# Kernel optimization log

Measured on AMD Instinct MI355X. Metric: run time of the kernel, lower is better.

Reference implementation:

```python
import jax, jax.numpy as jnp
import numpy as np

N_NODES = 20000   # N
N_EDGES = 320000  # E (avg degree 16)
T_STEPS = 16      # T
IN_FEATS = 1      # F
HG = 64           # hidden_g
HT = 128          # hidden_t
LN_EPS = 1e-5


def _layer_norm(x, g, b):
    mu = jnp.mean(x, axis=-1, keepdims=True)
    var = jnp.mean((x - mu) ** 2, axis=-1, keepdims=True)
    return (x - mu) * jax.lax.rsqrt(var + LN_EPS) * g + b


def setup_inputs() -> dict:
    key = jax.random.key(0)
    k = jax.random.split(key, 16)
    r = lambda i, shape, s: jax.random.normal(k[i], shape, jnp.float32) * s
    return dict(
        x_seq=jax.random.normal(k[0], (1, T_STEPS, N_NODES, IN_FEATS), jnp.float32),
        edge_index=jax.random.randint(k[1], (2, N_EDGES), 0, N_NODES, dtype=jnp.int32),
        # SAGEConv layer 0: lin_l (aggregated neighbors, has bias) + lin_r (root)
        W_l0=r(2, (IN_FEATS, HG), 0.5), W_r0=r(3, (IN_FEATS, HG), 0.5), b0=jnp.zeros((HG,), jnp.float32),
        ln0_g=jnp.ones((HG,), jnp.float32), ln0_b=jnp.zeros((HG,), jnp.float32),
        # SAGEConv layer 1
        W_l1=r(4, (HG, HG), 0.1), W_r1=r(5, (HG, HG), 0.1), b1=jnp.zeros((HG,), jnp.float32),
        ln1_g=jnp.ones((HG,), jnp.float32), ln1_b=jnp.zeros((HG,), jnp.float32),
        # GRU (torch layout: gates r,z,n stacked along first dim)
        gru_Wih=r(6, (3 * HT, HG), 0.05), gru_Whh=r(7, (3 * HT, HT), 0.05),
        gru_bih=jnp.zeros((3 * HT,), jnp.float32), gru_bhh=jnp.zeros((3 * HT,), jnp.float32),
        # head
        head_W=r(8, (HT, 1), 0.05), head_b=jnp.zeros((1,), jnp.float32),
    )


def reference(x_seq, edge_index, W_l0, W_r0, b0, ln0_g, ln0_b,
              W_l1, W_r1, b1, ln1_g, ln1_b,
              gru_Wih, gru_Whh, gru_bih, gru_bhh, head_W, head_b):
    src, dst = edge_index[0], edge_index[1]
    # in-degree for mean aggregation (clamped to 1, like PyG mean aggr on isolated nodes)
    deg = jnp.clip(jax.ops.segment_sum(jnp.ones((N_EDGES,), jnp.float32), dst,
                                       num_segments=N_NODES), 1.0)[:, None]

    def sage(x, Wl, Wr, b):
        # mean over incoming neighbors, then lin_l(aggr) + lin_r(root)
        agg = jax.ops.segment_sum(x[src], dst, num_segments=N_NODES) / deg
        return agg @ Wl + x @ Wr + b

    def stack(xt):  # xt: (N, F) -> (N, HG); dropout is identity in eval mode
        h = jax.nn.relu(_layer_norm(sage(xt, W_l0, W_r0, b0), ln0_g, ln0_b))
        h = jax.nn.relu(_layer_norm(sage(h, W_l1, W_r1, b1), ln1_g, ln1_b))
        return h

    X = x_seq[0]  # (T, N, F), B == 1
    # scan over timesteps (matches the per-t Python loop, bounds peak memory)
    _, H = jax.lax.scan(lambda c, xt: (c, stack(xt)), None, X)  # H: (T, N, HG)

    def gru_step(h, xt):  # torch GRU cell; batch = N nodes
        gi = xt @ gru_Wih.T + gru_bih
        gh = h @ gru_Whh.T + gru_bhh
        ir, iz, inn = jnp.split(gi, 3, axis=-1)
        hr, hz, hn = jnp.split(gh, 3, axis=-1)
        r = jax.nn.sigmoid(ir + hr)
        z = jax.nn.sigmoid(iz + hz)
        n = jnp.tanh(inn + r * hn)
        return (1.0 - z) * n + z * h, None

    h0 = jnp.zeros((N_NODES, HT), x_seq.dtype)
    hT, _ = jax.lax.scan(gru_step, h0, H)
    y = (hT @ head_W + head_b)[:, 0]  # (N,)
    return y
```

## Files before the change

### kernel.cpp

```cpp
#include <hip/hip_runtime.h>
#include <math.h>

#define NN 20000
#define NE 320000
#define TS 16
#define HG 64
#define HTT 128
#define NG 384
#define LN_EPS 1e-5f
#define ASTR 1032

typedef __attribute__((ext_vector_type(8))) _Float16 f16x8;
typedef __attribute__((ext_vector_type(4))) float f32x4;

__device__ __forceinline__ float wave_sum64(float v) {
  #pragma unroll
  for (int off = 32; off > 0; off >>= 1) v += __shfl_xor(v, off, 64);
  return v;
}
__device__ __forceinline__ float quad_sum16(float v) {
  #pragma unroll
  for (int off = 1; off < 16; off <<= 1) v += __shfl_xor(v, off, 64);
  return v;
}
__device__ __forceinline__ float fast_sigmoid(float x) {
  return __builtin_amdgcn_rcpf(1.f + __expf(-x));
}
__device__ __forceinline__ float fast_tanh(float x) {
  float e = __expf(-2.f * fabsf(x));
  float th = (1.f - e) * __builtin_amdgcn_rcpf(1.f + e);
  return copysignf(th, x);
}

__global__ __launch_bounds__(256) void k_setup(
    const float* __restrict__ x_seq, float* __restrict__ xT,
    const float* __restrict__ Wih, _Float16* __restrict__ WihF,
    const float* __restrict__ Whh, _Float16* __restrict__ WhhF,
    const float* __restrict__ Wl1, const float* __restrict__ Wr1,
    _Float16* __restrict__ Wchi, _Float16* __restrict__ Wclo,
    const float* __restrict__ Wl0, const float* __restrict__ Wr0,
    const float* __restrict__ b0, const float* __restrict__ g0,
    const float* __restrict__ be0, float* __restrict__ P,
    int* __restrict__ cnt, _Float16* __restrict__ h0r) {
  int gid = blockIdx.x * 256 + threadIdx.x;
  int stride = gridDim.x * 256;
  for (int i = gid; i < NN * TS; i += stride) {
    int t = i / NN, n = i - t * NN;
    xT[n * 16 + t] = x_seq[i];
  }
  for (int i = gid; i < NG * HG; i += stride) WihF[i] = (_Float16)Wih[i];
  for (int i = gid; i < NG * HTT; i += stride) WhhF[i] = (_Float16)Whh[i];
  for (int i = gid; i < HG * 128; i += stride) {
    int n = i >> 7, k = i & 127;
    float x = (k < HG) ? Wl1[k * HG + n] : Wr1[(k - HG) * HG + n];
    _Float16 h = (_Float16)x;
    Wchi[i] = h;
    Wclo[i] = (_Float16)(x - (float)h);
  }
  for (int i = gid; i < NN; i += stride) cnt[i] = 0;
  for (int i = gid; i < 1024; i += stride) h0r[(size_t)NN * 1024 + i] = (_Float16)0.f;
  if (blockIdx.x == 0 && threadIdx.x < 64) {
    int f = threadIdx.x;
    float u = Wl0[f], v = Wr0[f], c = b0[f], g = g0[f];
    float um = wave_sum64(u) * (1.f / 64.f);
    float vm = wave_sum64(v) * (1.f / 64.f);
    float cm = wave_sum64(c) * (1.f / 64.f);
    float uc = u - um, vc = v - vm, cc = c - cm;
    float muu = wave_sum64(uc * uc) * (1.f / 64.f);
    float mvv = wave_sum64(vc * vc) * (1.f / 64.f);
    float mcc = wave_sum64(cc * cc) * (1.f / 64.f);
    float muv = wave_sum64(uc * vc) * (1.f / 64.f);
    float muc = wave_sum64(uc * cc) * (1.f / 64.f);
    float mvc = wave_sum64(vc * cc) * (1.f / 64.f);
    P[f] = uc * g; P[64 + f] = vc * g; P[128 + f] = cc * g; P[192 + f] = be0[f];
    if (f == 0) {
      P[256] = muu; P[257] = mvv; P[258] = mcc;
      P[259] = muv; P[260] = muc; P[261] = mvc;
    }
  }
}

__global__ void k_hist(const int* __restrict__ dst, int* cnt) {
  int e = blockIdx.x * blockDim.x + threadIdx.x;
  if (e < NE) atomicAdd(&cnt[dst[e]], 1);
}

__global__ void k_scan(int* cnt, int* row_ptr, float* deg_inv) {
  __shared__ int s[1024];
  const int PER = 20;
  int tid = threadIdx.x;
  int base = tid * PER;
  int vloc[PER], dloc[PER];
  int sum = 0;
  #pragma unroll
  for (int j = 0; j < PER; j++) {
    int n = base + j;
    int d = (n < NN) ? cnt[n] : 0;
    vloc[j] = sum;
    dloc[j] = d;
    sum += d;
  }
  s[tid] = sum;
  __syncthreads();
  for (int off = 1; off < 1024; off <<= 1) {
    int t = (tid >= off) ? s[tid - off] : 0;
    __syncthreads();
    s[tid] += t;
    __syncthreads();
  }
  int excl = s[tid] - sum;
  #pragma unroll
  for (int j = 0; j < PER; j++) {
    int n = base + j;
    if (n < NN) {
      int rp = excl + vloc[j];
      row_ptr[n] = rp;
      cnt[n] = rp;
      int d = dloc[j];
      deg_inv[n] = 1.0f / (float)((d > 1) ? d : 1);
    }
  }
  if (tid == 1023) row_ptr[NN] = s[1023];
}

__global__ void k_fill(const int* __restrict__ src, const int* __restrict__ dst,
                       int* cursor, int* col) {
  int e = blockIdx.x * blockDim.x + threadIdx.x;
  if (e < NE) {
    int p = atomicAdd(&cursor[dst[e]], 1);
    col[p] = src[e];
  }
}

__global__ __launch_bounds__(256) void k_h0_fused(
    const float* __restrict__ xT,
    const int* __restrict__ row_ptr, const int* __restrict__ col,
    const float* __restrict__ deg_inv,
    const float* __restrict__ P,
    _Float16* __restrict__ h0r) {
  int lane = threadIdx.x & 63;
  int n = blockIdx.x * 4 + (threadIdx.x >> 6);
  int grp = lane >> 4, tl = lane & 15;
  int beg = row_ptr[n];
  int deg = row_ptr[n + 1] - beg;
  float s0 = 0.f, s1 = 0.f;
  int iters = (deg + 7) >> 3;
  for (int it = 0; it < iters; it++) {
    int e0 = it * 8 + grp, e1 = it * 8 + 4 + grp;
    bool v0 = e0 < deg, v1 = e1 < deg;
    int i0 = v0 ? e0 : 0, i1 = v1 ? e1 : 0;
    int c0 = col[beg + i0];
    int c1 = col[beg + i1];
    float x0 = xT[c0 * 16 + tl];
    float x1 = xT[c1 * 16 + tl];
    s0 += v0 ? x0 : 0.f;
    s1 += v1 ? x1 : 0.f;
  }
  float s = s0 + s1;
  s += __shfl_xor(s, 16, 64);
  s += __shfl_xor(s, 32, 64);
  float aggv = s * deg_inv[n];
  float xv = xT[n * 16 + tl];
  float muu = P[256], mvv = P[257], mcc = P[258];
  float muv = P[259], muc = P[260], mvc = P[261];
  #pragma unroll
  for (int half = 0; half < 2; half++) {
    int c = lane + half * 64;
    int t = c >> 3, f8 = (c & 7) * 8;
    float a = __shfl(aggv, t, 64);
    float x = __shfl(xv, t, 64);
    float var = a * a * muu + x * x * mvv + mcc
              + 2.f * (a * x * muv + a * muc + x * mvc);
    float rstd = rsqrtf(var + LN_EPS);
    f16x8 o;
    #pragma unroll
    for (int j = 0; j < 8; j++) {
      int f = f8 + j;
      float d = a * P[f] + x * P[64 + f] + P[128 + f];
      o[j] = (_Float16)fmaxf(d * rstd + P[192 + f], 0.f);
    }
    *(f16x8*)&h0r[(size_t)n * 1024 + c * 8] = o;
  }
}

__global__ __launch_bounds__(256) void k_sage_fused(
    const _Float16* __restrict__ h0r,
    const int* __restrict__ row_ptr, const int* __restrict__ col,
    const float* __restrict__ deg_inv,
    const _Float16* __restrict__ Wchi, const _Float16* __restrict__ Wclo,
    const float* __restrict__ b1, const float* __restrict__ g1, const float* __restrict__ be1,
    _Float16* __restrict__ Ht_all) {
  __shared__ _Float16 aggL[16 * ASTR];
  int tid = threadIdx.x;
  int lane = tid & 63, wave = tid >> 6;
  int col16 = lane & 15, quad = lane >> 4;
  int m0 = blockIdx.x * 16;
  (void)deg_inv;

  {
    int i4 = lane >> 4;
    int slot = lane & 15;
    int ni = m0 + wave * 4 + i4;
    int beg_i = row_ptr[ni];
    int d_i = row_ptr[ni + 1] - beg_i;
    int cv0 = (slot < d_i) ? col[beg_i + slot] : NN;
    int cv1 = (slot + 16 < d_i) ? col[beg_i + 16 + slot] : NN;

    int dL[4], bgL[4];
    #pragma unroll
    for (int i = 0; i < 4; i++) {
      dL[i] = __builtin_amdgcn_readlane(d_i, i << 4);
      bgL[i] = __builtin_amdgcn_readlane(beg_i, i << 4);
    }
    int dmax = dL[0];
    #pragma unroll
    for (int i = 1; i < 4; i++) if (dL[i] > dmax) dmax = dL[i];

    const f16x8 z = {0, 0, 0, 0, 0, 0, 0, 0};
    f16x8 aH[4] = {z, z, z, z}, aLo[4] = {z, z, z, z};

    int emax1 = (dmax < 16) ? dmax : 16;
    for (int e = 0; e < emax1; e += 2) {
      f16x8 tA[4], tB[4], tC[4], tD[4];
      #pragma unroll
      for (int i = 0; i < 4; i++) {
        int c0 = __builtin_amdgcn_readlane(cv0, (i << 4) | e);
        int c1 = __builtin_amdgcn_readlane(cv0, (i << 4) | (e + 1));
        const f16x8* p0 = (const f16x8*)(h0r + (size_t)c0 * 1024);
        const f16x8* p1 = (const f16x8*)(h0r + (size_t)c1 * 1024);
        tA[i] = p0[lane]; tB[i] = p0[lane + 64];
        tC[i] = p1[lane]; tD[i] = p1[lane + 64];
      }
      #pragma unroll
      for (int i = 0; i < 4; i++) {
        aH[i]  += tA[i] + tC[i];
        aLo[i] += tB[i] + tD[i];
      }
    }
    if (dmax > 16) {
      int emax2 = (dmax < 32) ? dmax : 32;
      for (int e = 16; e < emax2; e += 2) {
        f16x8 tA[4], tB[4], tC[4], tD[4];
        #pragma unroll
        for (int i = 0; i < 4; i++) {
          int c0 = __builtin_amdgcn_readlane(cv1, (i << 4) | (e - 16));
          int c1 = __builtin_amdgcn_readlane(cv1, (i << 4) | (e - 15));
          const f16x8* p0 = (const f16x8*)(h0r + (size_t)c0 * 1024);
          const f16x8* p1 = (const f16x8*)(h0r + (size_t)c1 * 1024);
          tA[i] = p0[lane]; tB[i] = p0[lane + 64];
          tC[i] = p1[lane]; tD[i] = p1[lane + 64];
        }
        #pragma unroll
        for (int i = 0; i < 4; i++) {
          aH[i]  += tA[i] + tC[i];
          aLo[i] += tB[i] + tD[i];
        }
      }
      if (dmax > 32) {
        #pragma unroll
        for (int i = 0; i < 4; i++) {
          for (int e = 32; e < dL[i]; e++) {
            int c = col[bgL[i] + e];
            const f16x8* p = (const f16x8*)(h0r + (size_t)c * 1024);
            aH[i]  += p[lane];
            aLo[i] += p[lane + 64];
          }
        }
      }
    }

    #pragma unroll
    for (int i = 0; i < 4; i++) {
      int dd = dL[i];
      float di = 1.0f / (float)((dd > 1) ? dd : 1);
      f16x8 o0, o1;
      #pragma unroll
      for (int j = 0; j < 8; j++) {
        o0[j] = (_Float16)((float)aH[i][j] * di);
        o1[j] = (_Float16)((float)aLo[i][j] * di);
      }
      int nl = wave * 4 + i;
      *(f16x8*)&aggL[nl * ASTR + lane * 8] = o0;
      *(f16x8*)&aggL[nl * ASTR + 512 + lane * 8] = o1;
    }
  }
  __syncthreads();

  for (int ts = 0; ts < 4; ts++) {
    int t = wave * 4 + ts;
    f32x4 acc[4];
    #pragma unroll
    for (int nt = 0; nt < 4; nt++) acc[nt] = (f32x4){0.f, 0.f, 0.f, 0.f};

    #pragma unroll
    for (int kk = 0; kk < 2; kk++) {
      f16x8 ah = *(const f16x8*)&aggL[col16 * ASTR + t * 64 + kk * 32 + quad * 8];
      #pragma unroll
      for (int nt = 0; nt < 4; nt++) {
        int nf = nt * 16 + col16;
        f16x8 bh = *(const f16x8*)&Wchi[nf * 128 + kk * 32 + quad * 8];
        f16x8 bl = *(const f16x8*)&Wclo[nf * 128 + kk * 32 + quad * 8];
        acc[nt] = __builtin_amdgcn_mfma_f32_16x16x32_f16(ah, bh, acc[nt], 0, 0, 0);
        acc[nt] = __builtin_amdgcn_mfma_f32_16x16x32_f16(ah, bl, acc[nt], 0, 0, 0);
      }
    }
    #pragma unroll
    for (int kk = 0; kk < 2; kk++) {
      f16x8 ah = *(const f16x8*)&h0r[(size_t)(m0 + col16) * 1024 + t * 64 + kk * 32 + quad * 8];
      #pragma unroll
      for (int nt = 0; nt < 4; nt++) {
        int nf = nt * 16 + col16;
        f16x8 bh = *(const f16x8*)&Wchi[nf * 128 + 64 + kk * 32 + quad * 8];
        f16x8 bl = *(const f16x8*)&Wclo[nf * 128 + 64 + kk * 32 + quad * 8];
        acc[nt] = __builtin_amdgcn_mfma_f32_16x16x32_f16(ah, bh, acc[nt], 0, 0, 0);
        acc[nt] = __builtin_amdgcn_mfma_f32_16x16x32_f16(ah, bl, acc[nt], 0, 0, 0);
      }
    }

    float bias[4], gg[4], bb[4];
    #pragma unroll
    for (int nt = 0; nt < 4; nt++) {
      int nf = nt * 16 + col16;
      bias[nt] = b1[nf]; gg[nt] = g1[nf]; bb[nt] = be1[nf];
    }
    #pragma unroll
    for (int r = 0; r < 4; r++) {
      float v[4];
      #pragma unroll
      for (int nt = 0; nt < 4; nt++) v[nt] = acc[nt][r] + bias[nt];
      float s = (v[0] + v[1]) + (v[2] + v[3]);
      float mu = quad_sum16(s) * (1.f / 64.f);
      float sq = 0.f;
      #pragma unroll
      for (int nt = 0; nt < 4; nt++) { v[nt] -= mu; sq += v[nt] * v[nt]; }
      float var = quad_sum16(sq) * (1.f / 64.f);
      float rstd = rsqrtf(var + LN_EPS);
      int m = m0 + quad * 4 + r;
      size_t base = ((size_t)t * NN + m) * HG;
      #pragma unroll
      for (int nt = 0; nt < 4; nt++) {
        float o = fmaxf(v[nt] * rstd * gg[nt] + bb[nt], 0.f);
        Ht_all[base + nt * 16 + col16] = (_Float16)o;
      }
    }
  }
}

__global__ __launch_bounds__(256, 2) void k_gru_all(
    const _Float16* __restrict__ Ht_all,
    const _Float16* __restrict__ WihF,
    const _Float16* __restrict__ WhhF,
    const float* __restrict__ bih, const float* __restrict__ bhh,
    const float* __restrict__ headW, const float* __restrict__ headb,
    float* __restrict__ out) {
  __shared__ _Float16 WihL[NG * 64];
  __shared__ _Float16 hL[2][32 * 128];
  __shared__ float yL[4][32];

  int tid = threadIdx.x;
  int lane = tid & 63, wave = tid >> 6;
  int col16 = lane & 15, quad = lane >> 4;
  int m0 = blockIdx.x * 32;
  int gb = 2 * wave;

  for (int i = tid; i < NG * 8; i += 256) {
    int g = i >> 3, k8 = i & 7;
    *(f16x8*)&WihL[g * 64 + ((k8 + g) & 7) * 8] = *(const f16x8*)&WihF[g * 64 + k8 * 8];
  }
  for (int i = tid; i < 2 * 32 * 128; i += 256) hL[0][i] = (_Float16)0.f;

  int gts[6];
  #pragma unroll
  for (int t6 = 0; t6 < 6; t6++)
    gts[t6] = (t6 < 2) ? (gb + t6) : (t6 < 4) ? (8 + gb + t6 - 2) : (16 + gb + t6 - 4);

  f16x8 wgh[4][6];
  #pragma unroll
  for (int kk = 0; kk < 4; kk++)
    #pragma unroll
    for (int t6 = 0; t6 < 6; t6++)
      wgh[kk][t6] = *(const f16x8*)&WhhF[(size_t)(gts[t6] * 16 + col16) * HTT + kk * 32 + quad * 8];

  int jj[2]; float bR[2], bZ[2], bNi[2], bNh[2], hw[2];
  int waddr[2][4][2];
  #pragma unroll
  for (int js = 0; js < 2; js++) {
    int j = (gb + js) * 16 + col16;
    jj[js] = j;
    bR[js]  = bih[j] + bhh[j];
    bZ[js]  = bih[HTT + j] + bhh[HTT + j];
    bNi[js] = bih[2 * HTT + j];
    bNh[js] = bhh[2 * HTT + j];
    hw[js]  = headW[j];
    #pragma unroll
    for (int mt = 0; mt < 2; mt++)
      #pragma unroll
      for (int r = 0; r < 4; r++) {
        int row = mt * 16 + quad * 4 + r;
        waddr[mt][r][js] = row * 128 + (((j >> 3) + row) & 15) * 8 + (j & 7);
      }
  }
  float hreg[2][4][2];
  #pragma unroll
  for (int mt = 0; mt < 2; mt++)
    #pragma unroll
    for (int r = 0; r < 4; r++) { hreg[mt][r][0] = 0.f; hreg[mt][r][1] = 0.f; }

  size_t aoff[2][2];
  #pragma unroll
  for (int kk = 0; kk < 2; kk++)
    #pragma unroll
    for (int mt = 0; mt < 2; mt++)
      aoff[kk][mt] = (size_t)(m0 + mt * 16 + col16) * HG + kk * 32 + quad * 8;

  __syncthreads();

  for (int t = 0; t < TS; t++) {
    const _Float16* hcur = hL[t & 1];
    _Float16* hnxt = hL[(t + 1) & 1];

    f32x4 acc[8][2];
    #pragma unroll
    for (int a = 0; a < 8; a++) {
      acc[a][0] = (f32x4){0.f, 0.f, 0.f, 0.f};
      acc[a][1] = (f32x4){0.f, 0.f, 0.f, 0.f};
    }

    const _Float16* AH = Ht_all + (size_t)t * NN * HG;
    f16x8 gah[2][2];
    #pragma unroll
    for (int kk = 0; kk < 2; kk++)
      #pragma unroll
      for (int mt = 0; mt < 2; mt++)
        gah[kk][mt] = *(const f16x8*)&AH[aoff[kk][mt]];

    #pragma unroll
    for (int kk = 0; kk < 4; kk++) {
      f16x8 ah[2];
      #pragma unroll
      for (int mt = 0; mt < 2; mt++) {
        int row = mt * 16 + col16;
        int k8 = kk * 4 + quad;
        ah[mt] = *(const f16x8*)&hcur[row * 128 + ((k8 + row) & 15) * 8];
      }
      #pragma unroll
      for (int t6 = 0; t6 < 6; t6++) {
        int ai = (t6 < 4) ? t6 : t6 + 2;
        #pragma unroll
        for (int mt = 0; mt < 2; mt++)
          acc[ai][mt] = __builtin_amdgcn_mfma_f32_16x16x32_f16(ah[mt], wgh[kk][t6], acc[ai][mt], 0, 0, 0);
      }
    }
    #pragma unroll
    for (int kk = 0; kk < 2; kk++) {
      #pragma unroll
      for (int t6 = 0; t6 < 6; t6++) {
        int g = gts[t6] * 16 + col16;
        int k8 = kk * 4 + quad;
        f16x8 b = *(const f16x8*)&WihL[g * 64 + ((k8 + g) & 7) * 8];
        #pragma unroll
        for (int mt = 0; mt < 2; mt++)
          acc[t6][mt] = __builtin_amdgcn_mfma_f32_16x16x32_f16(gah[kk][mt], b, acc[t6][mt], 0, 0, 0);
      }
    }

    #pragma unroll
    for (int mt = 0; mt < 2; mt++) {
      #pragma unroll
      for (int r = 0; r < 4; r++) {
        #pragma unroll
        for (int js = 0; js < 2; js++) {
          float R  = acc[0 + js][mt][r] + bR[js];
          float Z  = acc[2 + js][mt][r] + bZ[js];
          float Ni = acc[4 + js][mt][r] + bNi[js];
          float Nh = acc[6 + js][mt][r] + bNh[js];
          float rg = fast_sigmoid(R);
          float zg = fast_sigmoid(Z);
          float nn = fast_tanh(Ni + rg * Nh);
          float hn = nn + zg * (hreg[mt][r][js] - nn);
          hreg[mt][r][js] = hn;
          hnxt[waddr[mt][r][js]] = (_Float16)hn;
        }
      }
    }
    __syncthreads();
  }

  #pragma unroll
  for (int mt = 0; mt < 2; mt++) {
    #pragma unroll
    for (int r = 0; r < 4; r++) {
      float py = hreg[mt][r][0] * hw[0] + hreg[mt][r][1] * hw[1];
      py = quad_sum16(py);
      if (col16 == 0) yL[wave][mt * 16 + quad * 4 + r] = py;
    }
  }
  __syncthreads();
  if (tid < 32)
    out[m0 + tid] = yL[0][tid] + yL[1][tid] + yL[2][tid] + yL[3][tid] + headb[0];
}

extern "C" void kernel_launch(void* const* d_in, const int* in_sizes, int n_in,
                              void* d_out, int out_size, void* d_ws, size_t ws_size,
                              hipStream_t stream) {
  const float* x_seq = (const float*)d_in[0];
  const int*   edge  = (const int*)d_in[1];
  const float* Wl0   = (const float*)d_in[2];
  const float* Wr0   = (const float*)d_in[3];
  const float* b0    = (const float*)d_in[4];
  const float* g0    = (const float*)d_in[5];
  const float* be0   = (const float*)d_in[6];
  const float* Wl1   = (const float*)d_in[7];
  const float* Wr1   = (const float*)d_in[8];
  const float* b1    = (const float*)d_in[9];
  const float* g1    = (const float*)d_in[10];
  const float* be1   = (const float*)d_in[11];
  const float* Wih   = (const float*)d_in[12];
  const float* Whh   = (const float*)d_in[13];
  const float* bih   = (const float*)d_in[14];
  const float* bhh   = (const float*)d_in[15];
  const float* headW = (const float*)d_in[16];
  const float* headb = (const float*)d_in[17];
  float* out = (float*)d_out;

  const int* srcp = edge;
  const int* dstp = edge + NE;

  char* ws = (char*)d_ws;
  size_t off = 0;
  auto alloc = [&](size_t bytes) -> void* {
    void* p = ws + off;
    off += (bytes + 255) & ~(size_t)255;
    return p;
  };
  int*   cnt     = (int*)alloc(NN * 4);
  int*   row_ptr = (int*)alloc((NN + 1) * 4);
  int*   col     = (int*)alloc(NE * 4);
  float* deg_inv = (float*)alloc(NN * 4);
  float* xT      = (float*)alloc((size_t)NN * TS * 4);
  float* P       = (float*)alloc(512 * 4);
  _Float16* h0r  = (_Float16*)alloc((size_t)(NN + 1) * 1024 * 2);
  _Float16* Ht_all = (_Float16*)alloc((size_t)TS * NN * HG * 2);
  _Float16* WihF = (_Float16*)alloc((size_t)NG * HG * 2);
  _Float16* WhhF = (_Float16*)alloc((size_t)NG * HTT * 2);
  _Float16* Wchi = (_Float16*)alloc((size_t)HG * 128 * 2);
  _Float16* Wclo = (_Float16*)alloc((size_t)HG * 128 * 2);
  (void)ws_size; (void)in_sizes; (void)n_in; (void)out_size;

  k_setup<<<1250, 256, 0, stream>>>(x_seq, xT, Wih, WihF, Whh, WhhF,
                                    Wl1, Wr1, Wchi, Wclo,
                                    Wl0, Wr0, b0, g0, be0, P, cnt, h0r);
  k_hist<<<(NE + 255) / 256, 256, 0, stream>>>(dstp, cnt);
  k_scan<<<1, 1024, 0, stream>>>(cnt, row_ptr, deg_inv);
  k_fill<<<(NE + 255) / 256, 256, 0, stream>>>(srcp, dstp, cnt, col);
  k_h0_fused<<<NN / 4, 256, 0, stream>>>(xT, row_ptr, col, deg_inv, P, h0r);
  k_sage_fused<<<NN / 16, 256, 0, stream>>>(h0r, row_ptr, col, deg_inv,
                                            Wchi, Wclo, b1, g1, be1, Ht_all);
  k_gru_all<<<NN / 32, 256, 0, stream>>>(Ht_all, WihF, WhhF, bih, bhh,
                                         headW, headb, out);
}
```

Before: 390.3 us.

## Gather compact per-node layer-0 codes and rebuild neighbor features in sage aggregation

Because layer 0 has a single input feature, each neighbor's 64-wide post-LayerNorm activation is fully determined by three scalars (a*rstd, x*rstd, rstd). k_h0_fused now writes these as a compact fp16 code per node and timestep. k_sage_fused gathers these codes instead of full 2KB h0 rows and recomputes relu(A*Pu+X*Pv+C*Pc+Pb) in registers before summing. This removes most gather bandwidth in the neighbor aggregation at the cost of extra FMA work per edge, and accumulation now happens in fp32 instead of fp16. h0r is still written and passed to k_sage_fused even though the aggregation no longer reads it.

```diff
diff --git a/kernel.cpp b/kernel.cpp
--- a/kernel.cpp
+++ b/kernel.cpp
@@ -11,6 +11,7 @@
 #define ASTR 1032
 
 typedef __attribute__((ext_vector_type(8))) _Float16 f16x8;
+typedef __attribute__((ext_vector_type(4))) _Float16 f16x4;
 typedef __attribute__((ext_vector_type(4))) float f32x4;
 
 __device__ __forceinline__ float wave_sum64(float v) {
@@ -41,7 +42,7 @@
     const float* __restrict__ Wl0, const float* __restrict__ Wr0,
     const float* __restrict__ b0, const float* __restrict__ g0,
     const float* __restrict__ be0, float* __restrict__ P,
-    int* __restrict__ cnt, _Float16* __restrict__ h0r) {
+    int* __restrict__ cnt) {
   int gid = blockIdx.x * 256 + threadIdx.x;
   int stride = gridDim.x * 256;
   for (int i = gid; i < NN * TS; i += stride) {
@@ -58,7 +59,6 @@
     Wclo[i] = (_Float16)(x - (float)h);
   }
   for (int i = gid; i < NN; i += stride) cnt[i] = 0;
-  for (int i = gid; i < 1024; i += stride) h0r[(size_t)NN * 1024 + i] = (_Float16)0.f;
   if (blockIdx.x == 0 && threadIdx.x < 64) {
     int f = threadIdx.x;
     float u = Wl0[f], v = Wr0[f], c = b0[f], g = g0[f];
@@ -137,7 +137,8 @@
     const int* __restrict__ row_ptr, const int* __restrict__ col,
     const float* __restrict__ deg_inv,
     const float* __restrict__ P,
-    _Float16* __restrict__ h0r) {
+    _Float16* __restrict__ h0r,
+    _Float16* __restrict__ code) {
   int lane = threadIdx.x & 63;
   int n = blockIdx.x * 4 + (threadIdx.x >> 6);
   int grp = lane >> 4, tl = lane & 15;
@@ -163,6 +164,18 @@
   float xv = xT[n * 16 + tl];
   float muu = P[256], mvv = P[257], mcc = P[258];
   float muv = P[259], muc = P[260], mvc = P[261];
+  if (lane < 16) {
+    float a = aggv, x = xv;
+    float var = a * a * muu + x * x * mvv + mcc
+              + 2.f * (a * x * muv + a * muc + x * mvc);
+    float rstd = rsqrtf(var + LN_EPS);
+    f16x4 cw;
+    cw[0] = (_Float16)(a * rstd);
+    cw[1] = (_Float16)(x * rstd);
+    cw[2] = (_Float16)rstd;
+    cw[3] = (_Float16)0.f;
+    *(f16x4*)&code[(size_t)n * 64 + (lane & 7) * 8 + (lane >> 3) * 4] = cw;
+  }
   #pragma unroll
   for (int half = 0; half < 2; half++) {
     int c = lane + half * 64;
@@ -186,7 +199,8 @@
 __global__ __launch_bounds__(256) void k_sage_fused(
     const _Float16* __restrict__ h0r,
     const int* __restrict__ row_ptr, const int* __restrict__ col,
-    const float* __restrict__ deg_inv,
+    const _Float16* __restrict__ code,
+    const float* __restrict__ P,
     const _Float16* __restrict__ Wchi, const _Float16* __restrict__ Wclo,
     const float* __restrict__ b1, const float* __restrict__ g1, const float* __restrict__ be1,
     _Float16* __restrict__ Ht_all) {
@@ -195,89 +209,93 @@
   int lane = tid & 63, wave = tid >> 6;
   int col16 = lane & 15, quad = lane >> 4;
   int m0 = blockIdx.x * 16;
-  (void)deg_inv;
 
   {
+    int f1 = (lane & 7) * 8;
+    float Pu[8], Pv[8], Pc[8], Pb[8];
+    #pragma unroll
+    for (int j = 0; j < 8; j++) {
+      Pu[j] = P[f1 + j];
+      Pv[j] = P[64 + f1 + j];
+      Pc[j] = P[128 + f1 + j];
+      Pb[j] = P[192 + f1 + j];
+    }
+    int codeoff = (lane >> 3) * 8;
+
     int i4 = lane >> 4;
     int slot = lane & 15;
     int ni = m0 + wave * 4 + i4;
     int beg_i = row_ptr[ni];
     int d_i = row_ptr[ni + 1] - beg_i;
-    int cv0 = (slot < d_i) ? col[beg_i + slot] : NN;
-    int cv1 = (slot + 16 < d_i) ? col[beg_i + 16 + slot] : NN;
-
+    int cv0 = (slot < d_i) ? col[beg_i + slot] : 0;
+    int cv1 = (slot + 16 < d_i) ? col[beg_i + 16 + slot] : 0;
     int dL[4], bgL[4];
     #pragma unroll
     for (int i = 0; i < 4; i++) {
       dL[i] = __builtin_amdgcn_readlane(d_i, i << 4);
       bgL[i] = __builtin_amdgcn_readlane(beg_i, i << 4);
     }
-    int dmax = dL[0];
-    #pragma unroll
-    for (int i = 1; i < 4; i++) if (dL[i] > dmax) dmax = dL[i];
-
-    const f16x8 z = {0, 0, 0, 0, 0, 0, 0, 0};
-    f16x8 aH[4] = {z, z, z, z}, aLo[4] = {z, z, z, z};
-
-    int emax1 = (dmax < 16) ? dmax : 16;
-    for (int e = 0; e < emax1; e += 2) {
-      f16x8 tA[4], tB[4], tC[4], tD[4];
-      #pragma unroll
-      for (int i = 0; i < 4; i++) {
+
+    for (int i = 0; i < 4; i++) {
+      float acc1[8], acc2[8];
+      #pragma unroll
+      for (int j = 0; j < 8; j++) { acc1[j] = 0.f; acc2[j] = 0.f; }
+
+      auto accum = [&](f16x8 cd) {
+        float A1 = (float)cd[0], X1 = (float)cd[1], C1 = (float)cd[2];
+        float A2 = (float)cd[4], X2 = (float)cd[5], C2 = (float)cd[6];
+        #pragma unroll
+        for (int j = 0; j < 8; j++) {
+          float d1 = fmaf(A1, Pu[j], fmaf(X1, Pv[j], fmaf(C1, Pc[j], Pb[j])));
+          acc1[j] += fmaxf(d1, 0.f);
+          float d2 = fmaf(A2, Pu[j], fmaf(X2, Pv[j], fmaf(C2, Pc[j], Pb[j])));
+          acc2[j] += fmaxf(d2, 0.f);
+        }
+      };
+      auto ldcode = [&](int c) -> f16x8 {
+        return *(const f16x8*)(code + (size_t)c * 64 + codeoff);
+      };
+
+      int deg = dL[i];
+      int m1 = (deg < 16) ? deg : 16;
+      int e = 0;
+      for (; e + 2 <= m1; e += 2) {
         int c0 = __builtin_amdgcn_readlane(cv0, (i << 4) | e);
         int c1 = __builtin_amdgcn_readlane(cv0, (i << 4) | (e + 1));
-        const f16x8* p0 = (const f16x8*)(h0r + (size_t)c0 * 1024);
-        const f16x8* p1 = (const f16x8*)(h0r + (size_t)c1 * 1024);
-        tA[i] = p0[lane]; tB[i] = p0[lane + 64];
-        tC[i] = p1[lane]; tD[i] = p1[lane + 64];
-      }
-      #pragma unroll
-      for (int i = 0; i < 4; i++) {
-        aH[i]  += tA[i] + tC[i];
-        aLo[i] += tB[i] + tD[i];
-      }
-    }
-    if (dmax > 16) {
-      int emax2 = (dmax < 32) ? dmax : 32;
-      for (int e = 16; e < emax2; e += 2) {
-        f16x8 tA[4], tB[4], tC[4], tD[4];
-        #pragma unroll
-        for (int i = 0; i < 4; i++) {
-          int c0 = __builtin_amdgcn_readlane(cv1, (i << 4) | (e - 16));
-          int c1 = __builtin_amdgcn_readlane(cv1, (i << 4) | (e - 15));
-          const f16x8* p0 = (const f16x8*)(h0r + (size_t)c0 * 1024);
-          const f16x8* p1 = (const f16x8*)(h0r + (size_t)c1 * 1024);
-          tA[i] = p0[lane]; tB[i] = p0[lane + 64];
-          tC[i] = p1[lane]; tD[i] = p1[lane + 64];
+        f16x8 cd0 = ldcode(c0);
+        f16x8 cd1 = ldcode(c1);
+        accum(cd0);
+        accum(cd1);
+      }
+      if (e < m1) {
+        int c0 = __builtin_amdgcn_readlane(cv0, (i << 4) | e);
+        accum(ldcode(c0));
+      }
+      if (deg > 16) {
+        int m2 = ((deg < 32) ? deg : 32) - 16;
+        e = 0;
+        for (; e + 2 <= m2; e += 2) {
+          int c0 = __builtin_amdgcn_readlane(cv1, (i << 4) | e);
+          int c1 = __builtin_amdgcn_readlane(cv1, (i << 4) | (e + 1));
+          f16x8 cd0 = ldcode(c0);
+          f16x8 cd1 = ldcode(c1);
+          accum(cd0);
+          accum(cd1);
         }
-        #pragma unroll
-        for (int i = 0; i < 4; i++) {
-          aH[i]  += tA[i] + tC[i];
-          aLo[i] += tB[i] + tD[i];
+        if (e < m2) {
+          int c0 = __builtin_amdgcn_readlane(cv1, (i << 4) | e);
+          accum(ldcode(c0));
         }
-      }
-      if (dmax > 32) {
-        #pragma unroll
-        for (int i = 0; i < 4; i++) {
-          for (int e = 32; e < dL[i]; e++) {
-            int c = col[bgL[i] + e];
-            const f16x8* p = (const f16x8*)(h0r + (size_t)c * 1024);
-            aH[i]  += p[lane];
-            aLo[i] += p[lane + 64];
-          }
-        }
-      }
-    }
-
-    #pragma unroll
-    for (int i = 0; i < 4; i++) {
-      int dd = dL[i];
-      float di = 1.0f / (float)((dd > 1) ? dd : 1);
+        for (int e3 = 32; e3 < deg; e3++)
+          accum(ldcode(col[bgL[i] + e3]));
+      }
+
+      float di = 1.0f / (float)((deg > 1) ? deg : 1);
       f16x8 o0, o1;
       #pragma unroll
       for (int j = 0; j < 8; j++) {
-        o0[j] = (_Float16)((float)aH[i][j] * di);
-        o1[j] = (_Float16)((float)aLo[i][j] * di);
+        o0[j] = (_Float16)(acc1[j] * di);
+        o1[j] = (_Float16)(acc2[j] * di);
       }
       int nl = wave * 4 + i;
       *(f16x8*)&aggL[nl * ASTR + lane * 8] = o0;
@@ -539,7 +557,8 @@
   float* deg_inv = (float*)alloc(NN * 4);
   float* xT      = (float*)alloc((size_t)NN * TS * 4);
   float* P       = (float*)alloc(512 * 4);
-  _Float16* h0r  = (_Float16*)alloc((size_t)(NN + 1) * 1024 * 2);
+  _Float16* h0r  = (_Float16*)alloc((size_t)NN * 1024 * 2);
+  _Float16* code = (_Float16*)alloc((size_t)NN * 64 * 2);
   _Float16* Ht_all = (_Float16*)alloc((size_t)TS * NN * HG * 2);
   _Float16* WihF = (_Float16*)alloc((size_t)NG * HG * 2);
   _Float16* WhhF = (_Float16*)alloc((size_t)NG * HTT * 2);
@@ -549,12 +568,12 @@
 
   k_setup<<<1250, 256, 0, stream>>>(x_seq, xT, Wih, WihF, Whh, WhhF,
                                     Wl1, Wr1, Wchi, Wclo,
-                                    Wl0, Wr0, b0, g0, be0, P, cnt, h0r);
+                                    Wl0, Wr0, b0, g0, be0, P, cnt);
   k_hist<<<(NE + 255) / 256, 256, 0, stream>>>(dstp, cnt);
   k_scan<<<1, 1024, 0, stream>>>(cnt, row_ptr, deg_inv);
   k_fill<<<(NE + 255) / 256, 256, 0, stream>>>(srcp, dstp, cnt, col);
-  k_h0_fused<<<NN / 4, 256, 0, stream>>>(xT, row_ptr, col, deg_inv, P, h0r);
-  k_sage_fused<<<NN / 16, 256, 0, stream>>>(h0r, row_ptr, col, deg_inv,
+  k_h0_fused<<<NN / 4, 256, 0, stream>>>(xT, row_ptr, col, deg_inv, P, h0r, code);
+  k_sage_fused<<<NN / 16, 256, 0, stream>>>(h0r, row_ptr, col, code, P,
                                             Wchi, Wclo, b1, g1, be1, Ht_all);
   k_gru_all<<<NN / 32, 256, 0, stream>>>(Ht_all, WihF, WhhF, bih, bhh,
                                          headW, headb, out);
```

Measured after the change: 387.8 us. No clear change (-0.6%).
